# Kernel tuning notes

Measured on AMD Instinct MI355X. Metric: run time of the kernel, lower is better.

## Reference

```python
import jax, jax.numpy as jnp
import numpy as np

B, S, H, A, M, V, E = 128, 64, 1000, 1000, 500, 30000, 620


def setup_inputs() -> dict:
    key = jax.random.key(0)
    ks = jax.random.split(key, 20)
    sc = 0.02
    return {
        "x": jax.random.randint(ks[0], (B, 1), 0, V),
        "hidden": jax.random.normal(ks[1], (B, H), jnp.float32),
        "outputs": jax.random.normal(ks[2], (B, S, 2 * H), jnp.float32),
        "emb": jax.random.normal(ks[3], (V, E), jnp.float32) * sc,
        "W_hp": jax.random.normal(ks[4], (A, H), jnp.float32) * sc,
        "b_hp": jnp.zeros((A,), jnp.float32),
        "W_op": jax.random.normal(ks[5], (A, 2 * H), jnp.float32) * sc,
        "b_op": jnp.zeros((A,), jnp.float32),
        "v_e": jax.random.normal(ks[6], (A,), jnp.float32) * sc,
        "W_ih": jax.random.normal(ks[7], (3 * H, 2 * H + E), jnp.float32) * sc,
        "W_hh": jax.random.normal(ks[8], (3 * H, H), jnp.float32) * sc,
        "b_ih": jnp.zeros((3 * H,), jnp.float32),
        "b_hh": jnp.zeros((3 * H,), jnp.float32),
        "W_wv": jax.random.normal(ks[9], (2 * M, 2 * H), jnp.float32) * sc,
        "b_wv": jnp.zeros((2 * M,), jnp.float32),
        "W_lh": jax.random.normal(ks[10], (2 * M, H), jnp.float32) * sc,
        "b_lh": jnp.zeros((2 * M,), jnp.float32),
        "W_le": jax.random.normal(ks[11], (2 * M, E), jnp.float32) * sc,
        "b_le": jnp.zeros((2 * M,), jnp.float32),
        "W_pred": jax.random.normal(ks[12], (V, M), jnp.float32) * sc,
        "b_pred": jnp.zeros((V,), jnp.float32),
    }


def reference(x, hidden, outputs, emb, W_hp, b_hp, W_op, b_op, v_e,
              W_ih, W_hh, b_ih, b_hh, W_wv, b_wv, W_lh, b_lh, W_le, b_le,
              W_pred, b_pred):
    # --- Bahdanau attention (broadcast instead of repeat) ---
    h_proj = hidden @ W_hp.T + b_hp                      # [B,A]
    o_proj = jnp.einsum('bsk,ak->bsa', outputs, W_op) + b_op  # [B,S,A]
    energy = jnp.tanh(h_proj[:, None, :] + o_proj) @ v_e # [B,S]
    attn = jax.nn.softmax(energy, axis=1)                # [B,S]
    ctx = jnp.einsum('bs,bsk->bk', attn, outputs)        # [B,2H] weighted_values

    # --- embedding lookup ---
    emb_x = emb[x[:, 0]]                                 # [B,E]

    # --- single-step GRU (PyTorch gate layout: r, z, n) ---
    gru_in = jnp.concatenate([emb_x, ctx], axis=1)       # [B, E+2H]
    gi = gru_in @ W_ih.T + b_ih                          # [B,3H]
    gh = hidden @ W_hh.T + b_hh                          # [B,3H]
    ir, iz, inn = gi[:, :H], gi[:, H:2*H], gi[:, 2*H:]
    hr, hz, hn = gh[:, :H], gh[:, H:2*H], gh[:, 2*H:]
    r = jax.nn.sigmoid(ir + hr)
    z = jax.nn.sigmoid(iz + hz)
    n = jnp.tanh(inn + r * hn)
    h_new = (1.0 - z) * n + z * hidden                   # [B,H]

    # --- maxout combine of three linears ---
    mo_in = (hidden @ W_lh.T + b_lh) + (emb_x @ W_le.T + b_le) + (ctx @ W_wv.T + b_wv)  # [B,2M]
    mo = mo_in.reshape(-1, M, 2).max(axis=2)             # [B,M]

    prediction = mo @ W_pred.T + b_pred                  # [B,V]
    return prediction, h_new
```

## Files before the change

kernel.cpp:

```cpp
#include <hip/hip_runtime.h>
#include <hip/hip_bf16.h>
#include <math.h>

typedef short bf16x8 __attribute__((ext_vector_type(8)));
typedef float f32x4 __attribute__((ext_vector_type(4)));
typedef unsigned short us8 __attribute__((ext_vector_type(8)));
typedef unsigned short us4 __attribute__((ext_vector_type(4)));

namespace {
constexpr int B_ = 128;
constexpr int S_ = 64;
constexpr int H_ = 1000;
constexpr int A_ = 1000;
constexpr int M_ = 500;
constexpr int V_ = 30000;
constexpr int E_ = 620;

constexpr int KP_OUT  = 2048;
constexpr int KP_HP   = 1024;
constexpr int KP_PRED = 512;
constexpr int LD_CAT  = 3712;
constexpr int NP_A    = 1024;
constexpr int NP_3H   = 3072;
constexpr int OROWS   = 8192;

constexpr int Z_HP = 4, Z_GI = 6, Z_GH = 4, Z_MO = 6, Z_OP = 2;

__device__ __forceinline__ unsigned short f2b(float f) {
  __hip_bfloat16 h = __float2bfloat16(f);
  return *reinterpret_cast<unsigned short*>(&h);
}
__device__ __forceinline__ float b2f(unsigned short u) {
  unsigned v = ((unsigned)u) << 16;
  return __uint_as_float(v);
}
__device__ __forceinline__ float sigmoidf_(float x) {
  return 1.0f / (1.0f + __expf(-x));
}
__device__ __forceinline__ void load_lds16(const void* g, void* l) {
  auto gp = reinterpret_cast<const __attribute__((address_space(1))) char*>(
      reinterpret_cast<uintptr_t>(g));
  unsigned loff = (unsigned)(uintptr_t)l;
  auto lp = reinterpret_cast<__attribute__((address_space(3))) char*>(loff);
  __builtin_amdgcn_global_load_lds(gp, lp, 16, 0, 0);
}
}

struct CJob {
  const float* src; unsigned short* dst;
  int nchunks, cpr, Kel, Rs, ld, coff, Wlim, bstart, nblk;
};

__global__ __launch_bounds__(256) void megacast(CJob j0, CJob j1, CJob j2)
{
  const int bid = blockIdx.x;
  CJob j = j0;
  if (bid >= j1.bstart) j = j1;
  if (bid >= j2.bstart) j = j2;

  const int tpj = j.nblk << 8;
  const int base = ((bid - j.bstart) << 8) + (int)threadIdx.x;

  for (int i = base; i < j.nchunks; i += tpj * 2) {
    const int i2 = i + tpj;
    const bool okB = (i2 < j.nchunks);
    const int rA = i / j.cpr;
    const int cA = (i - rA * j.cpr) << 3;
    const int rB = okB ? (i2 / j.cpr) : 0;
    const int cB = okB ? ((i2 - rB * j.cpr) << 3) : 0;
    const bool fA = (rA < j.Rs) && (cA + 8 <= j.Kel);
    const bool fB = okB && (rB < j.Rs) && (cB + 8 <= j.Kel);

    float4 a0, a1, b0, b1;
    if (fA) {
      const float* s = j.src + (size_t)rA * j.Kel + cA;
      a0 = *(const float4*)s; a1 = *(const float4*)(s + 4);
    }
    if (fB) {
      const float* s = j.src + (size_t)rB * j.Kel + cB;
      b0 = *(const float4*)s; b1 = *(const float4*)(s + 4);
    }

    if (fA) {
      us8 o;
      o[0] = f2b(a0.x); o[1] = f2b(a0.y); o[2] = f2b(a0.z); o[3] = f2b(a0.w);
      o[4] = f2b(a1.x); o[5] = f2b(a1.y); o[6] = f2b(a1.z); o[7] = f2b(a1.w);
      *(us8*)(j.dst + (size_t)rA * j.ld + j.coff + cA) = o;
    } else {
      unsigned short* drow = j.dst + (size_t)rA * j.ld + j.coff;
#pragma unroll
      for (int e = 0; e < 8; ++e) {
        const int c = cA + e;
        if (c < j.Wlim) {
          const float v = (rA < j.Rs && c < j.Kel)
                              ? j.src[(size_t)rA * j.Kel + c] : 0.f;
          drow[c] = f2b(v);
        }
      }
    }
    if (okB) {
      if (fB) {
        us8 o;
        o[0] = f2b(b0.x); o[1] = f2b(b0.y); o[2] = f2b(b0.z); o[3] = f2b(b0.w);
        o[4] = f2b(b1.x); o[5] = f2b(b1.y); o[6] = f2b(b1.z); o[7] = f2b(b1.w);
        *(us8*)(j.dst + (size_t)rB * j.ld + j.coff + cB) = o;
      } else {
        unsigned short* drow = j.dst + (size_t)rB * j.ld + j.coff;
#pragma unroll
        for (int e = 0; e < 8; ++e) {
          const int c = cB + e;
          if (c < j.Wlim) {
            const float v = (rB < j.Rs && c < j.Kel)
                                ? j.src[(size_t)rB * j.Kel + c] : 0.f;
            drow[c] = f2b(v);
          }
        }
      }
    }
  }
}

struct SJob {
  const unsigned short* A; int lda;
  const float* B; int ldb;
  int Nv, Kv;
  float* C; int ldc;
  const float* bias; int Ncol;
  int nK, Z, ntiles, bstart;
};

__global__ __launch_bounds__(256, 4) void gemm_skinny(
    SJob j0, SJob j1, SJob j2, SJob j3)
{
  __shared__ __align__(16) char Bs[2][4096];

  const int bid = blockIdx.x;
  SJob j = j0;
  if (bid >= j1.bstart) j = j1;
  if (bid >= j2.bstart) j = j2;
  if (bid >= j3.bstart) j = j3;
  const int lb = bid - j.bstart;
  const int tile = lb % j.ntiles, z = lb / j.ntiles;
  const int n0 = tile * 32;
  const int ks = (int)((long)j.nK * z / j.Z);
  const int ke = (int)((long)j.nK * (z + 1) / j.Z);

  const int t = threadIdx.x, lane = t & 63, wid = t >> 6;
  const int l15 = lane & 15, l4 = lane >> 4;
  const int mrow = (wid & 1) * 64;
  const int whalf = wid >> 1;

  const int srow = t >> 3;
  const int skq = (t & 7) * 8;
  const int grow = n0 + srow;
  const bool rowok = grow < j.Nv;
  const float* Bp = j.B + (size_t)(rowok ? grow : 0) * j.ldb;
  const unsigned swcol = (unsigned)(skq * 2) ^ (((unsigned)srow & 7u) << 4);

  const unsigned short* Arow = j.A + (size_t)(mrow + l15) * j.lda + l4 * 8;
  const int brow = whalf * 16 + l15;
  const unsigned bb = (unsigned)brow * 128;
  const unsigned bsw = (((unsigned)brow & 7u) << 4);

  float4 sf0, sf1;
  auto stage_load = [&](int kst) {
    const int gk = kst * 64 + skq;
    sf0 = make_float4(0.f, 0.f, 0.f, 0.f);
    sf1 = make_float4(0.f, 0.f, 0.f, 0.f);
    if (rowok) {
      if (gk + 8 <= j.Kv) {
        sf0 = *(const float4*)(Bp + gk);
        sf1 = *(const float4*)(Bp + gk + 4);
      } else {
        float tmp[8];
#pragma unroll
        for (int e = 0; e < 8; ++e)
          tmp[e] = (gk + e < j.Kv) ? Bp[gk + e] : 0.f;
        sf0 = make_float4(tmp[0], tmp[1], tmp[2], tmp[3]);
        sf1 = make_float4(tmp[4], tmp[5], tmp[6], tmp[7]);
      }
    }
  };
  auto stage_write = [&](int buf) {
    us8 o;
    o[0] = f2b(sf0.x); o[1] = f2b(sf0.y); o[2] = f2b(sf0.z); o[3] = f2b(sf0.w);
    o[4] = f2b(sf1.x); o[5] = f2b(sf1.y); o[6] = f2b(sf1.z); o[7] = f2b(sf1.w);
    *(us8*)((char*)Bs[buf] + srow * 128 + swcol) = o;
  };

  f32x4 acc[4] = {};
  stage_load(ks);
  stage_write(0);
  __syncthreads();

  for (int kst = ks; kst < ke; ++kst) {
    const int cur = (kst - ks) & 1;
    const bool more = (kst + 1 < ke);
    if (more) stage_load(kst + 1);
    bf16x8 Af[4][2];
#pragma unroll
    for (int kk = 0; kk < 2; ++kk)
#pragma unroll
      for (int mf = 0; mf < 4; ++mf)
        Af[mf][kk] = *(const bf16x8*)(Arow + (size_t)mf * 16 * j.lda +
                                      kst * 64 + kk * 32);
    bf16x8 Bf[2];
#pragma unroll
    for (int kk = 0; kk < 2; ++kk)
      Bf[kk] = *(const bf16x8*)((char*)Bs[cur] + bb +
                                ((unsigned)(kk * 64 + l4 * 16) ^ bsw));
#pragma unroll
    for (int kk = 0; kk < 2; ++kk)
#pragma unroll
      for (int mf = 0; mf < 4; ++mf)
        acc[mf] = __builtin_amdgcn_mfma_f32_16x16x32_bf16(Af[mf][kk], Bf[kk],
                                                          acc[mf], 0, 0, 0);
    if (more) stage_write(cur ^ 1);
    __syncthreads();
  }

  const int c = n0 + whalf * 16 + l15;
  if (j.bias) {
    if (c < j.Ncol) {
      const float bv = j.bias[c];
#pragma unroll
      for (int mf = 0; mf < 4; ++mf) {
        const int r = mrow + mf * 16 + l4 * 4;
#pragma unroll
        for (int q = 0; q < 4; ++q)
          j.C[(size_t)(r + q) * j.ldc + c] = acc[mf][q] + bv;
      }
    }
  } else {
    float* Cz = j.C + (size_t)z * 128 * j.ldc;
#pragma unroll
    for (int mf = 0; mf < 4; ++mf) {
      const int r = mrow + mf * 16 + l4 * 4;
#pragma unroll
      for (int q = 0; q < 4; ++q)
        Cz[(size_t)(r + q) * j.ldc + c] = acc[mf][q];
    }
  }
}

__global__ __launch_bounds__(256, 4) void pred_gemm(
    const unsigned short* __restrict__ mo_bf,
    const float* __restrict__ Wp,
    const float* __restrict__ bias,
    float* __restrict__ C)
{
  __shared__ __align__(16) char Bs[32768];

  const int t = threadIdx.x, lane = t & 63, wid = t >> 6;
  const int l15 = lane & 15, l4 = lane >> 4;
  const int n0 = blockIdx.x * 64;

  f32x4 acc[8] = {};

  for (int kb = 0; kb < 4; ++kb) {
#pragma unroll
    for (int i = 0; i < 8; ++i) {
      const unsigned off = (unsigned)t * 16 + (unsigned)i * 4096;
      const unsigned row = off >> 9, colb = off & 511u;
      const unsigned sc = colb ^ ((row & 7u) << 4);
      const int rg = n0 + (int)row;
      const unsigned kbyte = (unsigned)kb * 512 + sc;
      const bool ok = (rg < V_) && (kbyte + 16 <= 2000u);
      const char* src = ok ? ((const char*)Wp + (size_t)rg * 2000 + kbyte)
                           : (const char*)Wp;
      load_lds16(src, (char*)Bs + off);
    }
    __syncthreads();

#pragma unroll
    for (int ksl = 0; ksl < 4; ++ksl) {
      const unsigned br = (unsigned)wid * 16 + (unsigned)l15;
      const unsigned cb = ((unsigned)(ksl * 128 + l4 * 32)) ^ ((br & 7u) << 4);
      const float4 f0 = *(const float4*)(Bs + br * 512 + cb);
      const float4 f1 = *(const float4*)(Bs + br * 512 + (cb ^ 16u));
      bf16x8 bf;
      bf[0] = (short)f2b(f0.x); bf[1] = (short)f2b(f0.y);
      bf[2] = (short)f2b(f0.z); bf[3] = (short)f2b(f0.w);
      bf[4] = (short)f2b(f1.x); bf[5] = (short)f2b(f1.y);
      bf[6] = (short)f2b(f1.z); bf[7] = (short)f2b(f1.w);
#pragma unroll
      for (int mf = 0; mf < 8; ++mf) {
        const bf16x8 af = *(const bf16x8*)(mo_bf +
            (size_t)(mf * 16 + l15) * KP_PRED + kb * 128 + ksl * 32 + l4 * 8);
        acc[mf] = __builtin_amdgcn_mfma_f32_16x16x32_bf16(af, bf, acc[mf],
                                                          0, 0, 0);
      }
    }
    __syncthreads();
  }

  const int c = n0 + wid * 16 + l15;
  if (c < V_) {
    const float bv = bias[c];
#pragma unroll
    for (int mf = 0; mf < 8; ++mf) {
      const int r = mf * 16 + l4 * 4;
#pragma unroll
      for (int q = 0; q < 4; ++q)
        C[(size_t)(r + q) * V_ + c] = acc[mf][q] + bv;
    }
  }
}

__global__ __launch_bounds__(256, 4) void gemm128_part(
    const unsigned short* __restrict__ Abf, int ldA,
    const unsigned short* __restrict__ Bbf, int ldB,
    unsigned short* __restrict__ Cout, int ldc, int nK)
{
  __shared__ __align__(16) char As[16384];
  __shared__ __align__(16) char Bs[16384];

  const int t = threadIdx.x;
  const int lane = t & 63, wid = t >> 6;
  const int wm = wid >> 1, wn = wid & 1;
  const int l15 = lane & 15, l4 = lane >> 4;
  const int m0 = blockIdx.x * 128;
  const int n0 = blockIdx.y * 128;
  const int z = blockIdx.z, Z = gridDim.z;
  const int ks = (int)((long)nK * z / Z), ke = (int)((long)nK * (z + 1) / Z);

  f32x4 acc[4][4] = {};

  for (int kst = ks; kst < ke; ++kst) {
    const int k0 = kst * 64;
#pragma unroll
    for (int c = 0; c < 4; ++c) {
      const unsigned ou = c * 4096 + wid * 1024;
      const unsigned oo = ou + lane * 16;
      const unsigned row = oo >> 7, cb = oo & 127u;
      const unsigned scb = cb ^ ((row & 7u) << 4);
      load_lds16((const char*)Abf + ((size_t)(m0 + row) * ldA + k0) * 2 + scb,
                 As + ou);
    }
#pragma unroll
    for (int c = 0; c < 4; ++c) {
      const unsigned ou = c * 4096 + wid * 1024;
      const unsigned oo = ou + lane * 16;
      const unsigned row = oo >> 7, cb = oo & 127u;
      const unsigned scb = cb ^ ((row & 7u) << 4);
      load_lds16((const char*)Bbf + ((size_t)(n0 + row) * ldB + k0) * 2 + scb,
                 Bs + ou);
    }
    __syncthreads();

#pragma unroll
    for (int kk = 0; kk < 2; ++kk) {
      bf16x8 af[4], bfr[4];
#pragma unroll
      for (int i = 0; i < 4; ++i) {
        const unsigned ra = wm * 64 + i * 16 + l15;
        const unsigned ca = (unsigned)(kk * 64 + l4 * 16) ^ ((ra & 7u) << 4);
        af[i] = *(const bf16x8*)(As + ra * 128 + ca);
        const unsigned rb = wn * 64 + i * 16 + l15;
        const unsigned cb2 = (unsigned)(kk * 64 + l4 * 16) ^ ((rb & 7u) << 4);
        bfr[i] = *(const bf16x8*)(Bs + rb * 128 + cb2);
      }
#pragma unroll
      for (int i = 0; i < 4; ++i)
#pragma unroll
        for (int jj = 0; jj < 4; ++jj)
          acc[i][jj] = __builtin_amdgcn_mfma_f32_16x16x32_bf16(af[i], bfr[jj],
                                                               acc[i][jj], 0, 0, 0);
    }
    __syncthreads();
  }

  unsigned short* Cz = Cout + (size_t)z * OROWS * ldc;
#pragma unroll
  for (int i = 0; i < 4; ++i) {
    const int r = m0 + wm * 64 + i * 16 + l4 * 4;
#pragma unroll
    for (int jj = 0; jj < 4; ++jj) {
      const int c = n0 + wn * 64 + jj * 16 + l15;
#pragma unroll
      for (int q = 0; q < 4; ++q)
        Cz[(size_t)(r + q) * ldc + c] = f2b(acc[i][jj][q]);
    }
  }
}

__global__ __launch_bounds__(256) void hp_combine(
    const float* __restrict__ hp, const float* __restrict__ b_op,
    const float* __restrict__ b_hp, float* __restrict__ hpc)
{
  const int idx = blockIdx.x * 256 + threadIdx.x;
  if (idx >= B_ * NP_A) return;
  const int c = idx & (NP_A - 1);
  float s = (c < A_) ? (b_op[c] + b_hp[c]) : 0.f;
#pragma unroll
  for (int zz = 0; zz < Z_HP; ++zz) s += hp[(size_t)zz * B_ * NP_A + idx];
  hpc[idx] = s;
}

__global__ __launch_bounds__(256) void energy_reduce(
    const unsigned short* __restrict__ opart, const float* __restrict__ hpc,
    const float* __restrict__ ve, float* __restrict__ energy)
{
  const int r = blockIdx.x;
  const int b = r >> 6;
  const int t = threadIdx.x;
  float s = 0.f;
  if (t < 250) {
    const int c0 = t * 4;
    const us4 v0 = *(const us4*)(opart + (size_t)r * NP_A + c0);
    const us4 v1 = *(const us4*)(opart + (size_t)OROWS * NP_A + (size_t)r * NP_A + c0);
    const float4 h = *(const float4*)(hpc + (size_t)b * NP_A + c0);
    const float4 vv = *(const float4*)(ve + c0);
    s = tanhf(b2f(v0[0]) + b2f(v1[0]) + h.x) * vv.x
      + tanhf(b2f(v0[1]) + b2f(v1[1]) + h.y) * vv.y
      + tanhf(b2f(v0[2]) + b2f(v1[2]) + h.z) * vv.z
      + tanhf(b2f(v0[3]) + b2f(v1[3]) + h.w) * vv.w;
  }
#pragma unroll
  for (int w = 1; w < 64; w <<= 1) s += __shfl_xor(s, w);
  __shared__ float red[4];
  if ((t & 63) == 0) red[t >> 6] = s;
  __syncthreads();
  if (t == 0) energy[r] = red[0] + red[1] + red[2] + red[3];
}

__global__ __launch_bounds__(256) void softmax_ctx_cat(
    const float* __restrict__ energy, const unsigned short* __restrict__ outb,
    const float* __restrict__ hidden, const float* __restrict__ emb,
    const int* __restrict__ x, unsigned short* __restrict__ cat3)
{
  const int b = blockIdx.x, yq = blockIdx.y;
  const int t = threadIdx.x;
  __shared__ float attn[S_];
  __shared__ float sinv_s;

  if (t < 64) {
    const float e = energy[b * S_ + t];
    float m = e;
#pragma unroll
    for (int w = 1; w < 64; w <<= 1) m = fmaxf(m, __shfl_xor(m, w));
    const float p = __expf(e - m);
    float s = p;
#pragma unroll
    for (int w = 1; w < 64; w <<= 1) s += __shfl_xor(s, w);
    attn[t] = p;
    if (t == 0) sinv_s = 1.f / s;
  }
  __syncthreads();
  const float inv = sinv_s;
  unsigned short* catb = cat3 + (size_t)b * LD_CAT;

  {
    const int c0 = (250 * yq) / 4, c1 = (250 * (yq + 1)) / 4;
    const unsigned short* ob = outb + (size_t)b * S_ * KP_OUT;
    for (int kk = c0 + t; kk < c1; kk += 256) {
      float a[8] = {0.f, 0.f, 0.f, 0.f, 0.f, 0.f, 0.f, 0.f};
      for (int s = 0; s < S_; ++s) {
        const float w = attn[s];
        const us8 v = *(const us8*)(ob + (size_t)s * KP_OUT + kk * 8);
#pragma unroll
        for (int jj = 0; jj < 8; ++jj) a[jj] = fmaf(w, b2f(v[jj]), a[jj]);
      }
      us4 lo, hi;
#pragma unroll
      for (int jj = 0; jj < 4; ++jj) {
        lo[jj] = f2b(a[jj] * inv); hi[jj] = f2b(a[jj + 4] * inv);
      }
      *(us4*)(catb + 1620 + kk * 8) = lo;
      *(us4*)(catb + 1620 + kk * 8 + 4) = hi;
    }
  }
  {
    const int c0 = (250 * yq) / 4, c1 = (250 * (yq + 1)) / 4;
    for (int kk = c0 + t; kk < c1; kk += 256) {
      const float4 f = *(const float4*)(hidden + (size_t)b * H_ + kk * 4);
      us4 v; v[0] = f2b(f.x); v[1] = f2b(f.y); v[2] = f2b(f.z); v[3] = f2b(f.w);
      *(us4*)(catb + kk * 4) = v;
    }
  }
  {
    const int xi = x[b];
    const int c0 = (155 * yq) / 4, c1 = (155 * (yq + 1)) / 4;
    for (int kk = c0 + t; kk < c1; kk += 256) {
      const float4 f = *(const float4*)(emb + (size_t)xi * E_ + kk * 4);
      us4 v; v[0] = f2b(f.x); v[1] = f2b(f.y); v[2] = f2b(f.z); v[3] = f2b(f.w);
      *(us4*)(catb + 1000 + kk * 4) = v;
    }
  }
  if (yq == 3) {
    for (int kk = t; kk < 23; kk += 256) {
      us4 v; v[0] = 0; v[1] = 0; v[2] = 0; v[3] = 0;
      *(us4*)(catb + 3620 + kk * 4) = v;
    }
  }
}

__global__ __launch_bounds__(256) void gru_combine(
    const float* __restrict__ gi, const float* __restrict__ gh,
    const float* __restrict__ b_ih, const float* __restrict__ b_hh,
    const float* __restrict__ hidden, float* __restrict__ hout)
{
  const int idx = blockIdx.x * 256 + threadIdx.x;
  if (idx >= B_ * H_) return;
  const int b = idx / H_, h = idx - b * H_;
  float ir = b_ih[h], iz = b_ih[H_ + h], in = b_ih[2 * H_ + h];
  float hr = b_hh[h], hz = b_hh[H_ + h], hn = b_hh[2 * H_ + h];
#pragma unroll
  for (int zz = 0; zz < Z_GI; ++zz) {
    const float* g = gi + (size_t)zz * B_ * NP_3H + (size_t)b * NP_3H;
    ir += g[h]; iz += g[H_ + h]; in += g[2 * H_ + h];
  }
#pragma unroll
  for (int zz = 0; zz < Z_GH; ++zz) {
    const float* g = gh + (size_t)zz * B_ * NP_3H + (size_t)b * NP_3H;
    hr += g[h]; hz += g[H_ + h]; hn += g[2 * H_ + h];
  }
  const float r = sigmoidf_(ir + hr);
  const float zg = sigmoidf_(iz + hz);
  const float n = tanhf(in + r * hn);
  hout[idx] = (1.f - zg) * n + zg * hidden[idx];
}

__global__ __launch_bounds__(256) void maxpair_cast(
    const float* __restrict__ mo_in,
    const float* __restrict__ b_lh, const float* __restrict__ b_le,
    const float* __restrict__ b_wv, unsigned short* __restrict__ mo_bf)
{
  const int idx = blockIdx.x * 256 + threadIdx.x;
  if (idx >= B_ * KP_PRED) return;
  const int r = idx >> 9, c = idx & 511;
  unsigned short o = 0;
  if (c < M_) {
    const int j0 = 2 * c, j1 = 2 * c + 1;
    float v0 = b_lh[j0] + b_le[j0] + b_wv[j0];
    float v1 = b_lh[j1] + b_le[j1] + b_wv[j1];
#pragma unroll
    for (int zz = 0; zz < Z_MO; ++zz) {
      const float* g = mo_in + (size_t)zz * B_ * NP_A + (size_t)r * NP_A;
      v0 += g[j0]; v1 += g[j1];
    }
    o = f2b(fmaxf(v0, v1));
  }
  mo_bf[idx] = o;
}

extern "C" void kernel_launch(void* const* d_in, const int* in_sizes, int n_in,
                              void* d_out, int out_size, void* d_ws, size_t ws_size,
                              hipStream_t stream)
{
  const int*   x       = (const int*)  d_in[0];
  const float* hidden  = (const float*)d_in[1];
  const float* outputs = (const float*)d_in[2];
  const float* emb     = (const float*)d_in[3];
  const float* W_hp    = (const float*)d_in[4];
  const float* b_hp    = (const float*)d_in[5];
  const float* W_op    = (const float*)d_in[6];
  const float* b_op    = (const float*)d_in[7];
  const float* v_e     = (const float*)d_in[8];
  const float* W_ih    = (const float*)d_in[9];
  const float* W_hh    = (const float*)d_in[10];
  const float* b_ih    = (const float*)d_in[11];
  const float* b_hh    = (const float*)d_in[12];
  const float* W_wv    = (const float*)d_in[13];
  const float* b_wv    = (const float*)d_in[14];
  const float* W_lh    = (const float*)d_in[15];
  const float* b_lh    = (const float*)d_in[16];
  const float* W_le    = (const float*)d_in[17];
  const float* b_le    = (const float*)d_in[18];
  const float* W_pred  = (const float*)d_in[19];
  const float* b_pred  = (const float*)d_in[20];

  char* w = (char*)d_ws;
  auto alloc = [&](size_t bytes) {
    char* p = w; w += (bytes + 255) & ~(size_t)255; return p;
  };
  unsigned short* outputs_bf = (unsigned short*)alloc((size_t)OROWS * KP_OUT * 2);
  unsigned short* W_op_bf    = (unsigned short*)alloc((size_t)NP_A * KP_OUT * 2);
  unsigned short* hidden_bf  = (unsigned short*)alloc((size_t)B_ * KP_HP * 2);
  unsigned short* cat3_bf    = (unsigned short*)alloc((size_t)B_ * LD_CAT * 2);
  unsigned short* mo_bf      = (unsigned short*)alloc((size_t)B_ * KP_PRED * 2);
  float* hp     = (float*)alloc((size_t)Z_HP * B_ * NP_A * 4);
  float* hpc    = (float*)alloc((size_t)B_ * NP_A * 4);
  float* energy = (float*)alloc((size_t)B_ * S_ * 4);
  float* gh     = (float*)alloc((size_t)Z_GH * B_ * NP_3H * 4);
  char* un = w;
  unsigned short* opart = (unsigned short*)un;
  float* gi     = (float*)un;
  float* mo_in  = gi + (size_t)Z_GI * B_ * NP_3H;

  float* pred = (float*)d_out;
  float* hout = pred + (size_t)B_ * V_;

  const dim3 blk(256);
  const int FAR = 0x7fffffff;
  const SJob dummy = { nullptr, 0, nullptr, 0, 0, 0, nullptr, 0,
                       nullptr, 0, 1, 1, 1, FAR };

  {
    CJob jo  = { outputs, outputs_bf, OROWS * 256, 256, 2000, OROWS,
                 KP_OUT, 0, KP_OUT, 0,    2560 };
    CJob jwo = { W_op,    W_op_bf,    NP_A * 256,  256, 2000, A_,
                 KP_OUT, 0, KP_OUT, 2560, 320 };
    CJob jh  = { hidden,  hidden_bf,  B_ * 128,    128, 1000, B_,
                 KP_HP,  0, KP_HP,  2880, 32 };
    megacast<<<dim3(2912), blk, 0, stream>>>(jo, jwo, jh);
  }

  {
    SJob jhp = { hidden_bf, KP_HP, W_hp, H_, A_, H_, hp, NP_A,
                 nullptr, 0, 16, Z_HP, 32, 0 };
    SJob jgh = { hidden_bf, KP_HP, W_hh, H_, 3 * H_, H_, gh, NP_3H,
                 nullptr, 0, 16, Z_GH, 94, 128 };
    gemm_skinny<<<dim3(504), blk, 0, stream>>>(jhp, jgh, dummy, dummy);
  }
  hp_combine<<<dim3(B_ * NP_A / 256), blk, 0, stream>>>(hp, b_op, b_hp, hpc);

  gemm128_part<<<dim3(64, 8, Z_OP), blk, 0, stream>>>(
      outputs_bf, KP_OUT, W_op_bf, KP_OUT, opart, NP_A, KP_OUT / 64);

  energy_reduce<<<dim3(OROWS), blk, 0, stream>>>(opart, hpc, v_e, energy);

  softmax_ctx_cat<<<dim3(B_, 4), blk, 0, stream>>>(
      energy, outputs_bf, hidden, emb, x, cat3_bf);

  {
    SJob jgi = { cat3_bf + 1000, LD_CAT, W_ih, 2620, 3 * H_, 2620, gi, NP_3H,
                 nullptr, 0, 41, Z_GI, 94, 0 };
    SJob jlh = { cat3_bf, LD_CAT, W_lh, H_, A_, H_,
                 mo_in, NP_A, nullptr, 0, 16, 2, 32, 564 };
    SJob jle = { cat3_bf + 1000, LD_CAT, W_le, E_, A_, E_,
                 mo_in + (size_t)2 * B_ * NP_A, NP_A, nullptr, 0, 10, 1, 32, 628 };
    SJob jwv = { cat3_bf + 1620, LD_CAT, W_wv, 2 * H_, A_, 2 * H_,
                 mo_in + (size_t)3 * B_ * NP_A, NP_A, nullptr, 0, 32, 3, 32, 660 };
    gemm_skinny<<<dim3(756), blk, 0, stream>>>(jgi, jlh, jle, jwv);
  }

  gru_combine<<<dim3((B_ * H_ + 255) / 256), blk, 0, stream>>>(
      gi, gh, b_ih, b_hh, hidden, hout);

  maxpair_cast<<<dim3((B_ * KP_PRED + 255) / 256), blk, 0, stream>>>(
      mo_in, b_lh, b_le, b_wv, mo_bf);

  pred_gemm<<<dim3(469), blk, 0, stream>>>(mo_bf, W_pred, b_pred, pred);
}
```

Measured before the change: 183.8 us.

## Precast W_pred to bf16 inside extra blocks of the attention GEMM

Adds extra grid rows to the o_proj GEMM launch that convert W_pred from fp32 to a zero-padded bf16 buffer, running alongside the main GEMM blocks. pred_gemm then streams half the bytes and loads bf16 fragments straight from LDS, with no per-element conversion. This moves the fp32 read of W_pred off the tail kernel and overlaps it with the attention GEMM. The cost is an extra bf16 buffer written and read back, and possible contention with the GEMM for bandwidth and CUs.

```diff
diff --git a/kernel.cpp b/kernel.cpp
--- a/kernel.cpp
+++ b/kernel.cpp
@@ -22,6 +22,7 @@
 constexpr int LD_CAT  = 3712;
 constexpr int NP_A    = 1024;
 constexpr int NP_3H   = 3072;
+constexpr int NP_PRED = 30080;
 constexpr int OROWS   = 8192;
 
 constexpr int Z_HP = 4, Z_GI = 6, Z_GH = 4, Z_MO = 6, Z_OP = 2;
@@ -245,7 +246,7 @@
 
 __global__ __launch_bounds__(256, 4) void pred_gemm(
     const unsigned short* __restrict__ mo_bf,
-    const float* __restrict__ Wp,
+    const unsigned short* __restrict__ Wpbf,
     const float* __restrict__ bias,
     float* __restrict__ C)
 {
@@ -257,36 +258,27 @@
 
   f32x4 acc[8] = {};
 
-  for (int kb = 0; kb < 4; ++kb) {
+  for (int kb = 0; kb < 2; ++kb) {
 #pragma unroll
     for (int i = 0; i < 8; ++i) {
       const unsigned off = (unsigned)t * 16 + (unsigned)i * 4096;
       const unsigned row = off >> 9, colb = off & 511u;
       const unsigned sc = colb ^ ((row & 7u) << 4);
-      const int rg = n0 + (int)row;
-      const unsigned kbyte = (unsigned)kb * 512 + sc;
-      const bool ok = (rg < V_) && (kbyte + 16 <= 2000u);
-      const char* src = ok ? ((const char*)Wp + (size_t)rg * 2000 + kbyte)
-                           : (const char*)Wp;
+      const char* src = (const char*)Wpbf +
+          (size_t)(n0 + row) * 1024 + (unsigned)kb * 512 + sc;
       load_lds16(src, (char*)Bs + off);
     }
     __syncthreads();
 
 #pragma unroll
-    for (int ksl = 0; ksl < 4; ++ksl) {
+    for (int ksl = 0; ksl < 8; ++ksl) {
       const unsigned br = (unsigned)wid * 16 + (unsigned)l15;
-      const unsigned cb = ((unsigned)(ksl * 128 + l4 * 32)) ^ ((br & 7u) << 4);
-      const float4 f0 = *(const float4*)(Bs + br * 512 + cb);
-      const float4 f1 = *(const float4*)(Bs + br * 512 + (cb ^ 16u));
-      bf16x8 bf;
-      bf[0] = (short)f2b(f0.x); bf[1] = (short)f2b(f0.y);
-      bf[2] = (short)f2b(f0.z); bf[3] = (short)f2b(f0.w);
-      bf[4] = (short)f2b(f1.x); bf[5] = (short)f2b(f1.y);
-      bf[6] = (short)f2b(f1.z); bf[7] = (short)f2b(f1.w);
+      const unsigned cb = ((unsigned)(ksl * 64 + l4 * 16)) ^ ((br & 7u) << 4);
+      const bf16x8 bf = *(const bf16x8*)(Bs + br * 512 + cb);
 #pragma unroll
       for (int mf = 0; mf < 8; ++mf) {
         const bf16x8 af = *(const bf16x8*)(mo_bf +
-            (size_t)(mf * 16 + l15) * KP_PRED + kb * 128 + ksl * 32 + l4 * 8);
+            (size_t)(mf * 16 + l15) * KP_PRED + kb * 256 + ksl * 32 + l4 * 8);
         acc[mf] = __builtin_amdgcn_mfma_f32_16x16x32_bf16(af, bf, acc[mf],
                                                           0, 0, 0);
       }
@@ -310,10 +302,66 @@
 __global__ __launch_bounds__(256, 4) void gemm128_part(
     const unsigned short* __restrict__ Abf, int ldA,
     const unsigned short* __restrict__ Bbf, int ldB,
-    unsigned short* __restrict__ Cout, int ldc, int nK)
+    unsigned short* __restrict__ Cout, int ldc, int nK,
+    const float* __restrict__ Wp, unsigned short* __restrict__ Wpbf)
 {
   __shared__ __align__(16) char As[16384];
   __shared__ __align__(16) char Bs[16384];
+
+  if (blockIdx.y >= 8) {
+    const int flat = (int)blockIdx.x + 64 * ((int)blockIdx.y - 8) +
+                     256 * (int)blockIdx.z;
+    const int stride = 512 * 256;
+    const int nch = NP_PRED * 64;
+    for (int i = flat * 256 + (int)threadIdx.x; i < nch; i += stride * 2) {
+      const int i2 = i + stride;
+      const bool okB = (i2 < nch);
+      const int rA = i >> 6, cA = (i & 63) << 3;
+      const int rB = okB ? (i2 >> 6) : 0, cB = okB ? ((i2 & 63) << 3) : 0;
+      const bool fA = (rA < V_) && (cA + 8 <= M_);
+      const bool fB = okB && (rB < V_) && (cB + 8 <= M_);
+      float4 a0, a1, b0, b1;
+      if (fA) {
+        const float* s = Wp + (size_t)rA * M_ + cA;
+        a0 = *(const float4*)s; a1 = *(const float4*)(s + 4);
+      }
+      if (fB) {
+        const float* s = Wp + (size_t)rB * M_ + cB;
+        b0 = *(const float4*)s; b1 = *(const float4*)(s + 4);
+      }
+      if (fA) {
+        us8 o;
+        o[0] = f2b(a0.x); o[1] = f2b(a0.y); o[2] = f2b(a0.z); o[3] = f2b(a0.w);
+        o[4] = f2b(a1.x); o[5] = f2b(a1.y); o[6] = f2b(a1.z); o[7] = f2b(a1.w);
+        *(us8*)(Wpbf + (size_t)rA * KP_PRED + cA) = o;
+      } else {
+        unsigned short* drow = Wpbf + (size_t)rA * KP_PRED;
+#pragma unroll
+        for (int e = 0; e < 8; ++e) {
+          const int c = cA + e;
+          const float v = (rA < V_ && c < M_) ? Wp[(size_t)rA * M_ + c] : 0.f;
+          drow[c] = f2b(v);
+        }
+      }
+      if (okB) {
+        if (fB) {
+          us8 o;
+          o[0] = f2b(b0.x); o[1] = f2b(b0.y); o[2] = f2b(b0.z); o[3] = f2b(b0.w);
+          o[4] = f2b(b1.x); o[5] = f2b(b1.y); o[6] = f2b(b1.z); o[7] = f2b(b1.w);
+          *(us8*)(Wpbf + (size_t)rB * KP_PRED + cB) = o;
+        } else {
+          unsigned short* drow = Wpbf + (size_t)rB * KP_PRED;
+#pragma unroll
+          for (int e = 0; e < 8; ++e) {
+            const int c = cB + e;
+            const float v = (rB < V_ && c < M_) ? Wp[(size_t)rB * M_ + c] : 0.f;
+            drow[c] = f2b(v);
+          }
+        }
+      }
+    }
+    return;
+  }
 
   const int t = threadIdx.x;
   const int lane = t & 63, wid = t >> 6;
@@ -576,6 +624,7 @@
   };
   unsigned short* outputs_bf = (unsigned short*)alloc((size_t)OROWS * KP_OUT * 2);
   unsigned short* W_op_bf    = (unsigned short*)alloc((size_t)NP_A * KP_OUT * 2);
+  unsigned short* W_pred_bf  = (unsigned short*)alloc((size_t)NP_PRED * KP_PRED * 2);
   unsigned short* hidden_bf  = (unsigned short*)alloc((size_t)B_ * KP_HP * 2);
   unsigned short* cat3_bf    = (unsigned short*)alloc((size_t)B_ * LD_CAT * 2);
   unsigned short* mo_bf      = (unsigned short*)alloc((size_t)B_ * KP_PRED * 2);
@@ -615,8 +664,9 @@
   }
   hp_combine<<<dim3(B_ * NP_A / 256), blk, 0, stream>>>(hp, b_op, b_hp, hpc);
 
-  gemm128_part<<<dim3(64, 8, Z_OP), blk, 0, stream>>>(
-      outputs_bf, KP_OUT, W_op_bf, KP_OUT, opart, NP_A, KP_OUT / 64);
+  gemm128_part<<<dim3(64, 12, Z_OP), blk, 0, stream>>>(
+      outputs_bf, KP_OUT, W_op_bf, KP_OUT, opart, NP_A, KP_OUT / 64,
+      W_pred, W_pred_bf);
 
   energy_reduce<<<dim3(OROWS), blk, 0, stream>>>(opart, hpc, v_e, energy);
 
@@ -641,5 +691,5 @@
   maxpair_cast<<<dim3((B_ * KP_PRED + 255) / 256), blk, 0, stream>>>(
       mo_in, b_lh, b_le, b_wv, mo_bf);
 
-  pred_gemm<<<dim3(469), blk, 0, stream>>>(mo_bf, W_pred, b_pred, pred);
-}
+  pred_gemm<<<dim3(469), blk, 0, stream>>>(mo_bf, W_pred_bf, b_pred, pred);
+}
```

Measured after the change: 203.5 us. 1.11x slower.

## Retile prediction GEMM to 32 columns per block with a single full-K LDS load

Applied to the files above, without the earlier changes.

The prediction GEMM now gives each block 32 output columns instead of 64, doubling the grid to 938 blocks. Each block loads the whole 512-wide K slab of W_pred into 64KB of LDS in one pass, removing the four-step K loop and its barriers. The four waves are split into two row halves and two column groups. This gives more parallelism and overlap across blocks, at the cost of lower occupancy per CU (launch bound 2 instead of 4) and twice the reads of the A operand.

```diff
diff --git a/kernel.cpp b/kernel.cpp
--- a/kernel.cpp
+++ b/kernel.cpp
@@ -243,63 +243,64 @@
   }
 }
 
-__global__ __launch_bounds__(256, 4) void pred_gemm(
+__global__ __launch_bounds__(256, 2) void pred_gemm(
     const unsigned short* __restrict__ mo_bf,
     const float* __restrict__ Wp,
     const float* __restrict__ bias,
     float* __restrict__ C)
 {
-  __shared__ __align__(16) char Bs[32768];
+  __shared__ __align__(16) char Bs[65536];
 
   const int t = threadIdx.x, lane = t & 63, wid = t >> 6;
   const int l15 = lane & 15, l4 = lane >> 4;
-  const int n0 = blockIdx.x * 64;
-
-  f32x4 acc[8] = {};
-
-  for (int kb = 0; kb < 4; ++kb) {
-#pragma unroll
-    for (int i = 0; i < 8; ++i) {
-      const unsigned off = (unsigned)t * 16 + (unsigned)i * 4096;
-      const unsigned row = off >> 9, colb = off & 511u;
-      const unsigned sc = colb ^ ((row & 7u) << 4);
-      const int rg = n0 + (int)row;
-      const unsigned kbyte = (unsigned)kb * 512 + sc;
-      const bool ok = (rg < V_) && (kbyte + 16 <= 2000u);
-      const char* src = ok ? ((const char*)Wp + (size_t)rg * 2000 + kbyte)
-                           : (const char*)Wp;
-      load_lds16(src, (char*)Bs + off);
-    }
-    __syncthreads();
-
-#pragma unroll
-    for (int ksl = 0; ksl < 4; ++ksl) {
-      const unsigned br = (unsigned)wid * 16 + (unsigned)l15;
-      const unsigned cb = ((unsigned)(ksl * 128 + l4 * 32)) ^ ((br & 7u) << 4);
-      const float4 f0 = *(const float4*)(Bs + br * 512 + cb);
-      const float4 f1 = *(const float4*)(Bs + br * 512 + (cb ^ 16u));
-      bf16x8 bf;
-      bf[0] = (short)f2b(f0.x); bf[1] = (short)f2b(f0.y);
-      bf[2] = (short)f2b(f0.z); bf[3] = (short)f2b(f0.w);
-      bf[4] = (short)f2b(f1.x); bf[5] = (short)f2b(f1.y);
-      bf[6] = (short)f2b(f1.z); bf[7] = (short)f2b(f1.w);
-#pragma unroll
-      for (int mf = 0; mf < 8; ++mf) {
-        const bf16x8 af = *(const bf16x8*)(mo_bf +
-            (size_t)(mf * 16 + l15) * KP_PRED + kb * 128 + ksl * 32 + l4 * 8);
-        acc[mf] = __builtin_amdgcn_mfma_f32_16x16x32_bf16(af, bf, acc[mf],
-                                                          0, 0, 0);
-      }
-    }
-    __syncthreads();
-  }
-
-  const int c = n0 + wid * 16 + l15;
+  const int n0 = blockIdx.x * 32;
+  const int mrow = (wid & 1) * 64;
+  const int wc = (wid >> 1) * 16;
+
+#pragma unroll
+  for (int i = 0; i < 16; ++i) {
+    const unsigned off = (unsigned)i * 4096 + (unsigned)t * 16;
+    const unsigned row = off >> 11, colb = off & 2047u;
+    const unsigned sc = colb ^ ((row & 7u) << 4);
+    const int rg = n0 + (int)row;
+    const bool ok = (rg < V_) && (sc + 16 <= 2000u);
+    const char* src = ok ? ((const char*)Wp + (size_t)rg * 2000 + sc)
+                         : (const char*)Wp;
+    load_lds16(src, (char*)Bs + off);
+  }
+  __syncthreads();
+
+  f32x4 acc[4] = {};
+  const unsigned br = (unsigned)(wc + l15);
+  const unsigned sw = (br & 7u) << 4;
+  const char* Brow = Bs + br * 2048;
+  const unsigned short* Abase = mo_bf + (size_t)(mrow + l15) * KP_PRED + l4 * 8;
+
+#pragma unroll
+  for (int ksl = 0; ksl < 16; ++ksl) {
+    const unsigned base = (unsigned)(ksl * 128 + l4 * 32);
+    const float4 f0 = *(const float4*)(Brow + (base ^ sw));
+    const float4 f1 = *(const float4*)(Brow + ((base + 16) ^ sw));
+    bf16x8 bf;
+    bf[0] = (short)f2b(f0.x); bf[1] = (short)f2b(f0.y);
+    bf[2] = (short)f2b(f0.z); bf[3] = (short)f2b(f0.w);
+    bf[4] = (short)f2b(f1.x); bf[5] = (short)f2b(f1.y);
+    bf[6] = (short)f2b(f1.z); bf[7] = (short)f2b(f1.w);
+#pragma unroll
+    for (int mf = 0; mf < 4; ++mf) {
+      const bf16x8 af = *(const bf16x8*)(Abase + (size_t)mf * 16 * KP_PRED +
+                                         ksl * 32);
+      acc[mf] = __builtin_amdgcn_mfma_f32_16x16x32_bf16(af, bf, acc[mf],
+                                                        0, 0, 0);
+    }
+  }
+
+  const int c = n0 + wc + l15;
   if (c < V_) {
     const float bv = bias[c];
 #pragma unroll
-    for (int mf = 0; mf < 8; ++mf) {
-      const int r = mf * 16 + l4 * 4;
+    for (int mf = 0; mf < 4; ++mf) {
+      const int r = mrow + mf * 16 + l4 * 4;
 #pragma unroll
       for (int q = 0; q < 4; ++q)
         C[(size_t)(r + q) * V_ + c] = acc[mf][q] + bv;
@@ -641,5 +642,5 @@
   maxpair_cast<<<dim3((B_ * KP_PRED + 255) / 256), blk, 0, stream>>>(
       mo_in, b_lh, b_le, b_wv, mo_bf);
 
-  pred_gemm<<<dim3(469), blk, 0, stream>>>(mo_bf, W_pred, b_pred, pred);
-}
+  pred_gemm<<<dim3(938), blk, 0, stream>>>(mo_bf, W_pred, b_pred, pred);
+}
```

After: 178.8 us. 2.7% less time.
